# Performance work log

Measured on AMD Instinct MI355X. Metric: run time of the kernel, lower is better.

Reference implementation:

```python
import jax, jax.numpy as jnp
import numpy as np

EPS = 1e-12  # torch F.normalize eps


def setup_inputs() -> dict:
    key = jax.random.key(0)
    k1, k2, k3 = jax.random.split(key, 3)
    Bq, Lq, Bd, Ld, V, D = 32, 256, 32, 256, 768, 128
    qry_hidden = jax.random.normal(k1, (Bq, Lq, V), dtype=jnp.float32)
    doc_hidden = jax.random.normal(k2, (Bd, Ld, V), dtype=jnp.float32)
    W_tok = jax.random.normal(k3, (V, D), dtype=jnp.float32) * 0.02
    b_tok = jnp.zeros((D,), dtype=jnp.float32)
    qry_attention_mask = jnp.ones((Bq, Lq), dtype=jnp.int32)
    return {
        "qry_hidden": qry_hidden,
        "doc_hidden": doc_hidden,
        "W_tok": W_tok,
        "b_tok": b_tok,
        "qry_attention_mask": qry_attention_mask,
    }


def _tok_reps(hidden, W_tok, b_tok):
    # tok_proj + L2 normalize over feature dim (dim=2)
    r = hidden @ W_tok + b_tok
    norm = jnp.maximum(jnp.linalg.norm(r, axis=2, keepdims=True), EPS)
    return r / norm


def _mask_sep(mask):
    # zero out the [SEP] position (last 1 in each row)
    sep_pos = mask.sum(axis=1) - 1
    return mask.at[jnp.arange(mask.shape[0]), sep_pos].set(0)


def reference(qry_hidden, doc_hidden, W_tok, b_tok, qry_attention_mask):
    q = _tok_reps(qry_hidden, W_tok, b_tok)   # [Bq, Lq, D]
    d = _tok_reps(doc_hidden, W_tok, b_tok)   # [Bd, Ld, D]
    mask = _mask_sep(qry_attention_mask)      # [Bq, Lq]
    # cartesian token-level scores: [Bq, Lq, Bd, Ld], MaxSim over doc tokens
    scores = jnp.einsum("qld,bmd->qlbm", q, d).max(axis=3)  # [Bq, Lq, Bd]
    # masked sum over query tokens, skipping position 0 ([CLS])
    tok_scores = (scores * mask[:, :, None].astype(scores.dtype))[:, 1:].sum(axis=1)
    return tok_scores  # [Bq, Bd]
```

## Files before the change

### kernel.cpp

```cpp
#include <hip/hip_runtime.h>
#include <hip/hip_bf16.h>
#include <stdint.h>
#include <math.h>


#define BQ 32
#define LQ 256
#define V  768
#define DIM 128
#define NQ (BQ * LQ)
#define ND (BQ * LQ)

typedef short bf16x8 __attribute__((ext_vector_type(8)));
typedef float f32x4  __attribute__((ext_vector_type(4)));
typedef float f32x16 __attribute__((ext_vector_type(16)));
typedef float fvec4  __attribute__((ext_vector_type(4)));
typedef unsigned short us4 __attribute__((ext_vector_type(4)));

__device__ inline unsigned short f2bf(float f) {
  __hip_bfloat16 h = __float2bfloat16(f);
  unsigned short u;
  __builtin_memcpy(&u, &h, 2);
  return u;
}

__device__ inline void gload_lds16(const void* g, void* lds) {
  __builtin_amdgcn_global_load_lds(
      (const __attribute__((address_space(1))) void*)g,
      (__attribute__((address_space(3))) void*)lds, 16, 0, 0);
}

__global__ void prep_kernel(const float* __restrict__ W,
                            unsigned short* __restrict__ WT,
                            const int* __restrict__ mask,
                            float* __restrict__ wmask) {
  if (blockIdx.x < 384) {
    int idx = blockIdx.x * 256 + threadIdx.x;
    int n = idx & 127;
    int k = idx >> 7;
    float v = W[idx];
    int kg = k >> 6;
    int kc = k & 63;
    int wb = ((((kc >> 3) ^ (n & 7)) << 4) | ((kc & 7) << 1));
    *(unsigned short*)((char*)WT + (size_t)n * 1536 + kg * 128 + wb) = f2bf(v);
  } else {
    int b = blockIdx.x - 384, t = threadIdx.x;
    int m = mask[b * 256 + t];
    int s = m;
    #pragma unroll
    for (int off = 1; off < 64; off <<= 1) s += __shfl_xor(s, off, 64);
    __shared__ int ws[4];
    int w = t >> 6, l = t & 63;
    if (l == 0) ws[w] = s;
    __syncthreads();
    int total = ws[0] + ws[1] + ws[2] + ws[3];
    int sep = total - 1;
    float out = (t == 0 || t == sep) ? 0.0f : (float)m;
    wmask[b * 256 + t] = out;
  }
}

__launch_bounds__(256, 2)
__global__ void proj_kernel(const float* __restrict__ qh, const float* __restrict__ dh,
                            const unsigned short* __restrict__ WT,
                            const float* __restrict__ bias,
                            unsigned short* __restrict__ qrep,
                            unsigned short* __restrict__ drep) {
  __shared__ __align__(16) unsigned short At[2][32 * 64];
  __shared__ __align__(16) unsigned short Bt[2][128 * 64];
  __shared__ float sq[4][32];

  const int t = threadIdx.x;
  const int w = t >> 6;
  const int l = t & 63;
  const int lm = l & 15, lg = l >> 4;
  const int rowblk = blockIdx.x * 32;

  int arow[2], ac4[2];
  const float* asrc[2];
  #pragma unroll
  for (int p = 0; p < 2; p++) {
    int id = p * 256 + t;
    arow[p] = id >> 4;
    ac4[p] = id & 15;
    int row_g = rowblk + arow[p];
    asrc[p] = (row_g < NQ) ? (qh + (size_t)row_g * V)
                           : (dh + (size_t)(row_g - NQ) * V);
  }

  f32x4 acc[2][2];
  #pragma unroll
  for (int r = 0; r < 2; r++)
    #pragma unroll
    for (int c = 0; c < 2; c++)
      acc[r][c] = f32x4{0.f, 0.f, 0.f, 0.f};

  float bias_c[2];
  #pragma unroll
  for (int c = 0; c < 2; c++) bias_c[c] = bias[w * 32 + c * 16 + lm];

  fvec4 apref[2];
  #pragma unroll
  for (int p = 0; p < 2; p++) apref[p] = *(const fvec4*)(asrc[p] + ac4[p] * 4);
  #pragma unroll
  for (int i = 0; i < 4; i++) {
    int off = i * 4096 + t * 16;
    int n = off >> 7, inrow = off & 127;
    gload_lds16((const char*)WT + (size_t)n * 1536 + inrow,
                (char*)Bt[0] + i * 4096 + w * 1024);
  }
  #pragma unroll
  for (int p = 0; p < 2; p++) {
    us4 b4;
    #pragma unroll
    for (int j = 0; j < 4; j++) b4[j] = f2bf(apref[p][j]);
    int wb = ((((ac4[p] >> 1) ^ (arow[p] & 7)) << 4) | ((ac4[p] & 1) << 3));
    *(us4*)((char*)At[0] + arow[p] * 128 + wb) = b4;
  }
  __syncthreads();

  for (int kk = 0; kk < 12; kk++) {
    const int cur = kk & 1;
    if (kk < 11) {
      #pragma unroll
      for (int p = 0; p < 2; p++)
        apref[p] = *(const fvec4*)(asrc[p] + (kk + 1) * 64 + ac4[p] * 4);
      #pragma unroll
      for (int i = 0; i < 4; i++) {
        int off = i * 4096 + t * 16;
        int n = off >> 7, inrow = off & 127;
        gload_lds16((const char*)WT + (size_t)n * 1536 + (kk + 1) * 128 + inrow,
                    (char*)Bt[cur ^ 1] + i * 4096 + w * 1024);
      }
    }
    #pragma unroll
    for (int ks = 0; ks < 2; ks++) {
      bf16x8 af[2], bfr[2];
      #pragma unroll
      for (int r = 0; r < 2; r++) {
        int row = r * 16 + lm;
        int ch = (ks * 4 + lg) ^ (row & 7);
        af[r] = *(const bf16x8*)((char*)At[cur] + row * 128 + ch * 16);
      }
      #pragma unroll
      for (int c = 0; c < 2; c++) {
        int n = w * 32 + c * 16 + lm;
        int ch = (ks * 4 + lg) ^ (n & 7);
        bfr[c] = *(const bf16x8*)((char*)Bt[cur] + n * 128 + ch * 16);
      }
      #pragma unroll
      for (int r = 0; r < 2; r++)
        #pragma unroll
        for (int c = 0; c < 2; c++)
          acc[r][c] = __builtin_amdgcn_mfma_f32_16x16x32_bf16(af[r], bfr[c], acc[r][c], 0, 0, 0);
    }
    if (kk < 11) {
      #pragma unroll
      for (int p = 0; p < 2; p++) {
        us4 b4;
        #pragma unroll
        for (int j = 0; j < 4; j++) b4[j] = f2bf(apref[p][j]);
        int wb = ((((ac4[p] >> 1) ^ (arow[p] & 7)) << 4) | ((ac4[p] & 1) << 3));
        *(us4*)((char*)At[cur ^ 1] + arow[p] * 128 + wb) = b4;
      }
    }
    __syncthreads();
  }

  float vout[2][2][4];
  float ss[2][4];
  #pragma unroll
  for (int r = 0; r < 2; r++) {
    #pragma unroll
    for (int j = 0; j < 4; j++) {
      float s = 0.f;
      #pragma unroll
      for (int c = 0; c < 2; c++) {
        float v = acc[r][c][j] + bias_c[c];
        vout[r][c][j] = v;
        s += v * v;
      }
      #pragma unroll
      for (int m = 1; m < 16; m <<= 1) s += __shfl_xor(s, m, 64);
      ss[r][j] = s;
    }
  }
  if (lm == 0) {
    #pragma unroll
    for (int r = 0; r < 2; r++)
      #pragma unroll
      for (int j = 0; j < 4; j++)
        sq[w][r * 16 + lg * 4 + j] = ss[r][j];
  }
  __syncthreads();
  #pragma unroll
  for (int r = 0; r < 2; r++) {
    #pragma unroll
    for (int j = 0; j < 4; j++) {
      int rowl = r * 16 + lg * 4 + j;
      float tot = sq[0][rowl] + sq[1][rowl] + sq[2][rowl] + sq[3][rowl];
      float inv = 1.0f / fmaxf(sqrtf(tot), 1e-12f);
      int row_g = rowblk + rowl;
      unsigned short* rep = (row_g < NQ) ? qrep : drep;
      int rl = (row_g < NQ) ? row_g : row_g - NQ;
      #pragma unroll
      for (int c = 0; c < 2; c++) {
        int col = w * 32 + c * 16 + lm;
        int byteoff = rl * 256 + ((((col >> 3) ^ (rl & 15)) << 4) | ((col & 7) << 1));
        *(unsigned short*)((char*)rep + byteoff) = f2bf(vout[r][c][j] * inv);
      }
    }
  }
}

__launch_bounds__(512, 2)
__global__ void score_kernel(const unsigned short* __restrict__ qrep,
                             const unsigned short* __restrict__ drep,
                             const float* __restrict__ wmask,
                             float* __restrict__ out) {
  __shared__ __align__(16) char smem[131072];
  char* Qt  = smem;
  char* Dt0 = smem + 65536;
  char* Dt1 = smem + 98304;
  float* maxAll   = (float*)smem;
  float* partial2 = (float*)(smem + 8192);

  const int t = threadIdx.x;
  const int w = t >> 6, l = t & 63;
  const int col = l & 31, hi = l >> 5;
  const int wr = w >> 2, wc = w & 3;
  const int qb = blockIdx.x;
  const int dg = blockIdx.y;

  const char* qsrc = (const char*)qrep + (size_t)qb * 65536;
  const char* dsrc = (const char*)drep + (size_t)dg * 262144;

  #pragma unroll
  for (int i = 0; i < 8; i++)
    gload_lds16(qsrc + i * 8192 + t * 16, Qt + i * 8192 + w * 1024);
  #pragma unroll
  for (int i = 0; i < 4; i++)
    gload_lds16(dsrc + i * 8192 + t * 16, Dt0 + i * 8192 + w * 1024);
  __syncthreads();

  bf16x8 qf[2][8];
  #pragma unroll
  for (int c = 0; c < 2; c++) {
    int n = wc * 64 + c * 32 + col;
    const char* rowb = Qt + n * 256;
    #pragma unroll
    for (int ks = 0; ks < 8; ks++) {
      int ch = (ks * 2 + hi) ^ (n & 15);
      qf[c][ks] = *(const bf16x8*)(rowb + ch * 16);
    }
  }

  f32x16 acc[2][2];
  float vmax[2] = {-INFINITY, -INFINITY};

  for (int db = 0; db < 4; db++) {
    {
      const char* nsrc = dsrc + (size_t)(2 * db + 1) * 32768;
      #pragma unroll
      for (int i = 0; i < 4; i++)
        gload_lds16(nsrc + i * 8192 + t * 16, Dt1 + i * 8192 + w * 1024);
    }
    #pragma unroll
    for (int r = 0; r < 2; r++)
      #pragma unroll
      for (int c = 0; c < 2; c++)
        #pragma unroll
        for (int g = 0; g < 16; g++) acc[r][c][g] = 0.f;
    #pragma unroll
    for (int ks = 0; ks < 8; ks++) {
      bf16x8 df[2];
      #pragma unroll
      for (int r = 0; r < 2; r++) {
        int m = wr * 64 + r * 32 + col;
        int ch = (ks * 2 + hi) ^ (m & 15);
        df[r] = *(const bf16x8*)(Dt0 + m * 256 + ch * 16);
      }
      #pragma unroll
      for (int r = 0; r < 2; r++)
        #pragma unroll
        for (int c = 0; c < 2; c++)
          acc[r][c] = __builtin_amdgcn_mfma_f32_32x32x16_bf16(df[r], qf[c][ks], acc[r][c], 0, 0, 0);
    }
    #pragma unroll
    for (int c = 0; c < 2; c++)
      #pragma unroll
      for (int r = 0; r < 2; r++)
        #pragma unroll
        for (int g = 0; g < 16; g++) vmax[c] = fmaxf(vmax[c], acc[r][c][g]);
    __syncthreads();

    if (db < 3) {
      const char* nsrc = dsrc + (size_t)(2 * db + 2) * 32768;
      #pragma unroll
      for (int i = 0; i < 4; i++)
        gload_lds16(nsrc + i * 8192 + t * 16, Dt0 + i * 8192 + w * 1024);
    }
    #pragma unroll
    for (int r = 0; r < 2; r++)
      #pragma unroll
      for (int c = 0; c < 2; c++)
        #pragma unroll
        for (int g = 0; g < 16; g++) acc[r][c][g] = 0.f;
    #pragma unroll
    for (int ks = 0; ks < 8; ks++) {
      bf16x8 df[2];
      #pragma unroll
      for (int r = 0; r < 2; r++) {
        int m = wr * 64 + r * 32 + col;
        int ch = (ks * 2 + hi) ^ (m & 15);
        df[r] = *(const bf16x8*)(Dt1 + m * 256 + ch * 16);
      }
      #pragma unroll
      for (int r = 0; r < 2; r++)
        #pragma unroll
        for (int c = 0; c < 2; c++)
          acc[r][c] = __builtin_amdgcn_mfma_f32_32x32x16_bf16(df[r], qf[c][ks], acc[r][c], 0, 0, 0);
    }
    #pragma unroll
    for (int c = 0; c < 2; c++)
      #pragma unroll
      for (int r = 0; r < 2; r++)
        #pragma unroll
        for (int g = 0; g < 16; g++) vmax[c] = fmaxf(vmax[c], acc[r][c][g]);

    #pragma unroll
    for (int c = 0; c < 2; c++) {
      float m = vmax[c];
      m = fmaxf(m, __shfl_xor(m, 32, 64));
      if (hi == 0) maxAll[db * 512 + wr * 256 + wc * 64 + c * 32 + col] = m;
      vmax[c] = -INFINITY;
    }
    __syncthreads();
  }

  {
    int db = w >> 1, h = w & 1;
    int tok0 = h * 128 + l;
    int tok1 = tok0 + 64;
    float m0 = fmaxf(maxAll[db * 512 + tok0], maxAll[db * 512 + 256 + tok0]);
    float m1 = fmaxf(maxAll[db * 512 + tok1], maxAll[db * 512 + 256 + tok1]);
    float contrib = m0 * wmask[qb * 256 + tok0] + m1 * wmask[qb * 256 + tok1];
    #pragma unroll
    for (int off = 1; off < 64; off <<= 1) contrib += __shfl_xor(contrib, off, 64);
    if (l == 0) partial2[w] = contrib;
  }
  __syncthreads();
  if (t < 4)
    out[qb * 32 + dg * 4 + t] = partial2[2 * t] + partial2[2 * t + 1];
}

extern "C" void kernel_launch(void* const* d_in, const int* in_sizes, int n_in,
                              void* d_out, int out_size, void* d_ws, size_t ws_size,
                              hipStream_t stream) {
  const float* qh  = (const float*)d_in[0];
  const float* dh  = (const float*)d_in[1];
  const float* W   = (const float*)d_in[2];
  const float* b   = (const float*)d_in[3];
  const int* mask  = (const int*)d_in[4];
  float* out = (float*)d_out;

  char* ws = (char*)d_ws;
  unsigned short* qrep = (unsigned short*)(ws);
  unsigned short* drep = (unsigned short*)(ws + (1 << 21));
  unsigned short* WT   = (unsigned short*)(ws + (1 << 22));
  float* wmaskp        = (float*)(ws + (1 << 22) + (192 << 10));

  prep_kernel<<<416, 256, 0, stream>>>(W, WT, mask, wmaskp);
  proj_kernel<<<512, 256, 0, stream>>>(qh, dh, WT, b, qrep, drep);
  score_kernel<<<dim3(32, 8), 512, 0, stream>>>(qrep, drep, wmaskp, out);
}
```

Measured before the change: 118.5 us.

## Fuse prep, projection and scoring into one cooperative kernel with grid syncs

Merges the three kernels into a single cooperative launch of 256 blocks of 512 threads, separated by grid-wide barriers, to remove launch gaps between stages. The projection phase is retiled so each block handles 64 rows with a 128-wide K step instead of 32 rows with 64. The weighted mask is now computed inline in the scoring phase, and the separate mask buffer is dropped. In exchange, grid syncs add barrier cost, and the projection stage now runs on fewer, larger blocks, which lowers parallelism for the memory-bound read of the fp32 hidden states.

New measurement: 187.3 us. +58.0%, slower.

```diff
diff --git a/kernel.cpp b/kernel.cpp
--- a/kernel.cpp
+++ b/kernel.cpp
@@ -1,8 +1,11 @@
 #include <hip/hip_runtime.h>
+#include <hip/hip_cooperative_groups.h>
 #include <hip/hip_bf16.h>
 #include <stdint.h>
 #include <math.h>
 
+
+namespace cg = cooperative_groups;
 
 #define BQ 32
 #define LQ 256
@@ -30,328 +33,328 @@
       (__attribute__((address_space(3))) void*)lds, 16, 0, 0);
 }
 
-__global__ void prep_kernel(const float* __restrict__ W,
-                            unsigned short* __restrict__ WT,
-                            const int* __restrict__ mask,
-                            float* __restrict__ wmask) {
-  if (blockIdx.x < 384) {
-    int idx = blockIdx.x * 256 + threadIdx.x;
-    int n = idx & 127;
-    int k = idx >> 7;
-    float v = W[idx];
-    int kg = k >> 6;
-    int kc = k & 63;
-    int wb = ((((kc >> 3) ^ (n & 7)) << 4) | ((kc & 7) << 1));
-    *(unsigned short*)((char*)WT + (size_t)n * 1536 + kg * 128 + wb) = f2bf(v);
-  } else {
-    int b = blockIdx.x - 384, t = threadIdx.x;
-    int m = mask[b * 256 + t];
-    int s = m;
-    #pragma unroll
-    for (int off = 1; off < 64; off <<= 1) s += __shfl_xor(s, off, 64);
-    __shared__ int ws[4];
-    int w = t >> 6, l = t & 63;
-    if (l == 0) ws[w] = s;
+__launch_bounds__(512, 2)
+__global__ void colbert_fused(const float* __restrict__ qh,
+                              const float* __restrict__ dh,
+                              const float* __restrict__ W,
+                              const float* __restrict__ bias,
+                              const int* __restrict__ mask,
+                              unsigned short* __restrict__ WT,
+                              unsigned short* __restrict__ qrep,
+                              unsigned short* __restrict__ drep,
+                              float* __restrict__ out) {
+  __shared__ __align__(16) char smem[131072];
+  const int t = threadIdx.x;
+  const int blk = blockIdx.x;
+  const int w = t >> 6, l = t & 63;
+
+  {
+    int idx = blk * 512 + t;
+    if (idx < 98304) {
+      int n = idx & 127, k = idx >> 7;
+      float v = W[idx];
+      int kg = k >> 6, kc = k & 63;
+      int wb = ((((kc >> 3) ^ (n & 7)) << 4) | ((kc & 7) << 1));
+      *(unsigned short*)((char*)WT + (size_t)n * 1536 + kg * 128 + wb) = f2bf(v);
+    }
+  }
+  cg::this_grid().sync();
+
+  {
+    char* At = smem;
+    char* Bt = smem + 32768;
+    float* sq = (float*)(smem + 98304);
+    const int lm = l & 15, lg = l >> 4;
+    const int wr2 = w >> 2, wc = w & 3;
+    const int rowblk = blk * 64;
+
+    int arow[4], ac4[4];
+    const float* asrc[4];
+    #pragma unroll
+    for (int p = 0; p < 4; p++) {
+      int id = p * 512 + t;
+      arow[p] = id >> 5;
+      ac4[p]  = id & 31;
+      int row_g = rowblk + arow[p];
+      asrc[p] = (row_g < NQ) ? (qh + (size_t)row_g * V)
+                             : (dh + (size_t)(row_g - NQ) * V);
+    }
+
+    f32x4 acc[2][2];
+    #pragma unroll
+    for (int r = 0; r < 2; r++)
+      #pragma unroll
+      for (int c = 0; c < 2; c++)
+        acc[r][c] = f32x4{0.f, 0.f, 0.f, 0.f};
+
+    float bias_c[2];
+    #pragma unroll
+    for (int c = 0; c < 2; c++) bias_c[c] = bias[wc * 32 + c * 16 + lm];
+
+    fvec4 ap[4];
+    #pragma unroll
+    for (int p = 0; p < 4; p++) ap[p] = *(const fvec4*)(asrc[p] + ac4[p] * 4);
+    #pragma unroll
+    for (int i = 0; i < 4; i++) {
+      int off = i * 8192 + t * 16;
+      int h = off >> 14, offh = off & 16383;
+      int n = offh >> 7, inr = offh & 127;
+      gload_lds16((const char*)WT + (size_t)n * 1536 + h * 128 + inr, Bt + off);
+    }
+    #pragma unroll
+    for (int p = 0; p < 4; p++) {
+      us4 b4;
+      #pragma unroll
+      for (int j = 0; j < 4; j++) b4[j] = f2bf(ap[p][j]);
+      int h = ac4[p] >> 4, kc4 = ac4[p] & 15;
+      int wb = ((((kc4 >> 1) ^ (arow[p] & 7)) << 4) | ((kc4 & 1) << 3));
+      *(us4*)(At + h * 8192 + arow[p] * 128 + wb) = b4;
+    }
     __syncthreads();
-    int total = ws[0] + ws[1] + ws[2] + ws[3];
-    int sep = total - 1;
-    float out = (t == 0 || t == sep) ? 0.0f : (float)m;
-    wmask[b * 256 + t] = out;
+
+    for (int kk = 0; kk < 6; kk++) {
+      const int cur = kk & 1;
+      char* curA = At + cur * 16384;
+      char* curB = Bt + (cur << 15);
+      if (kk < 5) {
+        #pragma unroll
+        for (int p = 0; p < 4; p++)
+          ap[p] = *(const fvec4*)(asrc[p] + (kk + 1) * 128 + ac4[p] * 4);
+        char* nxtB = Bt + ((cur ^ 1) << 15);
+        #pragma unroll
+        for (int i = 0; i < 4; i++) {
+          int off = i * 8192 + t * 16;
+          int h = off >> 14, offh = off & 16383;
+          int n = offh >> 7, inr = offh & 127;
+          gload_lds16((const char*)WT + (size_t)n * 1536 + ((kk + 1) * 2 + h) * 128 + inr,
+                      nxtB + off);
+        }
+      }
+      #pragma unroll
+      for (int ks = 0; ks < 4; ks++) {
+        const int h = ks >> 1, ksl = ks & 1;
+        bf16x8 af[2], bfr[2];
+        #pragma unroll
+        for (int r = 0; r < 2; r++) {
+          int row = wr2 * 32 + r * 16 + lm;
+          int ch = (ksl * 4 + lg) ^ (row & 7);
+          af[r] = *(const bf16x8*)(curA + h * 8192 + row * 128 + ch * 16);
+        }
+        #pragma unroll
+        for (int c = 0; c < 2; c++) {
+          int n = wc * 32 + c * 16 + lm;
+          int ch = (ksl * 4 + lg) ^ (n & 7);
+          bfr[c] = *(const bf16x8*)(curB + h * 16384 + n * 128 + ch * 16);
+        }
+        #pragma unroll
+        for (int r = 0; r < 2; r++)
+          #pragma unroll
+          for (int c = 0; c < 2; c++)
+            acc[r][c] = __builtin_amdgcn_mfma_f32_16x16x32_bf16(af[r], bfr[c], acc[r][c], 0, 0, 0);
+      }
+      if (kk < 5) {
+        char* nxtA = At + (cur ^ 1) * 16384;
+        #pragma unroll
+        for (int p = 0; p < 4; p++) {
+          us4 b4;
+          #pragma unroll
+          for (int j = 0; j < 4; j++) b4[j] = f2bf(ap[p][j]);
+          int h = ac4[p] >> 4, kc4 = ac4[p] & 15;
+          int wb = ((((kc4 >> 1) ^ (arow[p] & 7)) << 4) | ((kc4 & 1) << 3));
+          *(us4*)(nxtA + h * 8192 + arow[p] * 128 + wb) = b4;
+        }
+      }
+      __syncthreads();
+    }
+
+    float vout[2][2][4];
+    float ss[2][4];
+    #pragma unroll
+    for (int r = 0; r < 2; r++) {
+      #pragma unroll
+      for (int j = 0; j < 4; j++) {
+        float s = 0.f;
+        #pragma unroll
+        for (int c = 0; c < 2; c++) {
+          float v = acc[r][c][j] + bias_c[c];
+          vout[r][c][j] = v;
+          s += v * v;
+        }
+        #pragma unroll
+        for (int m = 1; m < 16; m <<= 1) s += __shfl_xor(s, m, 64);
+        ss[r][j] = s;
+      }
+    }
+    if (lm == 0) {
+      #pragma unroll
+      for (int r = 0; r < 2; r++)
+        #pragma unroll
+        for (int j = 0; j < 4; j++)
+          sq[wc * 64 + wr2 * 32 + r * 16 + lg * 4 + j] = ss[r][j];
+    }
+    __syncthreads();
+    #pragma unroll
+    for (int r = 0; r < 2; r++) {
+      #pragma unroll
+      for (int j = 0; j < 4; j++) {
+        int brow = wr2 * 32 + r * 16 + lg * 4 + j;
+        float tot = sq[brow] + sq[64 + brow] + sq[128 + brow] + sq[192 + brow];
+        float inv = 1.0f / fmaxf(sqrtf(tot), 1e-12f);
+        int row_g = rowblk + brow;
+        unsigned short* rep = (row_g < NQ) ? qrep : drep;
+        int rl = (row_g < NQ) ? row_g : row_g - NQ;
+        #pragma unroll
+        for (int c = 0; c < 2; c++) {
+          int col = wc * 32 + c * 16 + lm;
+          int byteoff = rl * 256 + ((((col >> 3) ^ (rl & 15)) << 4) | ((col & 7) << 1));
+          *(unsigned short*)((char*)rep + byteoff) = f2bf(vout[r][c][j] * inv);
+        }
+      }
+    }
   }
-}
-
-__launch_bounds__(256, 2)
-__global__ void proj_kernel(const float* __restrict__ qh, const float* __restrict__ dh,
-                            const unsigned short* __restrict__ WT,
-                            const float* __restrict__ bias,
-                            unsigned short* __restrict__ qrep,
-                            unsigned short* __restrict__ drep) {
-  __shared__ __align__(16) unsigned short At[2][32 * 64];
-  __shared__ __align__(16) unsigned short Bt[2][128 * 64];
-  __shared__ float sq[4][32];
-
-  const int t = threadIdx.x;
-  const int w = t >> 6;
-  const int l = t & 63;
-  const int lm = l & 15, lg = l >> 4;
-  const int rowblk = blockIdx.x * 32;
-
-  int arow[2], ac4[2];
-  const float* asrc[2];
-  #pragma unroll
-  for (int p = 0; p < 2; p++) {
-    int id = p * 256 + t;
-    arow[p] = id >> 4;
-    ac4[p] = id & 15;
-    int row_g = rowblk + arow[p];
-    asrc[p] = (row_g < NQ) ? (qh + (size_t)row_g * V)
-                           : (dh + (size_t)(row_g - NQ) * V);
+  cg::this_grid().sync();
+
+  {
+    char* Qt  = smem;
+    char* Dt0 = smem + 65536;
+    char* Dt1 = smem + 98304;
+    float* maxAll   = (float*)smem;
+    float* partial2 = (float*)(smem + 8192);
+
+    const int col = l & 31, hi = l >> 5;
+    const int wr = w >> 2, wc = w & 3;
+    const int qb = blk >> 3;
+    const int dg = blk & 7;
+
+    const char* qsrc = (const char*)qrep + (size_t)qb * 65536;
+    const char* dsrc = (const char*)drep + (size_t)dg * 262144;
+
+    #pragma unroll
+    for (int i = 0; i < 8; i++)
+      gload_lds16(qsrc + i * 8192 + t * 16, Qt + i * 8192 + w * 1024);
+    #pragma unroll
+    for (int i = 0; i < 4; i++)
+      gload_lds16(dsrc + i * 8192 + t * 16, Dt0 + i * 8192 + w * 1024);
+    __syncthreads();
+
+    bf16x8 qf[2][8];
+    #pragma unroll
+    for (int c = 0; c < 2; c++) {
+      int n = wc * 64 + c * 32 + col;
+      const char* rowb = Qt + n * 256;
+      #pragma unroll
+      for (int ks = 0; ks < 8; ks++) {
+        int ch = (ks * 2 + hi) ^ (n & 15);
+        qf[c][ks] = *(const bf16x8*)(rowb + ch * 16);
+      }
+    }
+
+    f32x16 acc[2][2];
+    float vmax[2] = {-INFINITY, -INFINITY};
+
+    for (int db = 0; db < 4; db++) {
+      {
+        const char* nsrc = dsrc + (size_t)(2 * db + 1) * 32768;
+        #pragma unroll
+        for (int i = 0; i < 4; i++)
+          gload_lds16(nsrc + i * 8192 + t * 16, Dt1 + i * 8192 + w * 1024);
+      }
+      #pragma unroll
+      for (int r = 0; r < 2; r++)
+        #pragma unroll
+        for (int c = 0; c < 2; c++)
+          #pragma unroll
+          for (int g = 0; g < 16; g++) acc[r][c][g] = 0.f;
+      #pragma unroll
+      for (int ks = 0; ks < 8; ks++) {
+        bf16x8 df[2];
+        #pragma unroll
+        for (int r = 0; r < 2; r++) {
+          int m = wr * 64 + r * 32 + col;
+          int ch = (ks * 2 + hi) ^ (m & 15);
+          df[r] = *(const bf16x8*)(Dt0 + m * 256 + ch * 16);
+        }
+        #pragma unroll
+        for (int r = 0; r < 2; r++)
+          #pragma unroll
+          for (int c = 0; c < 2; c++)
+            acc[r][c] = __builtin_amdgcn_mfma_f32_32x32x16_bf16(df[r], qf[c][ks], acc[r][c], 0, 0, 0);
+      }
+      #pragma unroll
+      for (int c = 0; c < 2; c++)
+        #pragma unroll
+        for (int r = 0; r < 2; r++)
+          #pragma unroll
+          for (int g = 0; g < 16; g++) vmax[c] = fmaxf(vmax[c], acc[r][c][g]);
+      __syncthreads();
+
+      if (db < 3) {
+        const char* nsrc = dsrc + (size_t)(2 * db + 2) * 32768;
+        #pragma unroll
+        for (int i = 0; i < 4; i++)
+          gload_lds16(nsrc + i * 8192 + t * 16, Dt0 + i * 8192 + w * 1024);
+      }
+      #pragma unroll
+      for (int r = 0; r < 2; r++)
+        #pragma unroll
+        for (int c = 0; c < 2; c++)
+          #pragma unroll
+          for (int g = 0; g < 16; g++) acc[r][c][g] = 0.f;
+      #pragma unroll
+      for (int ks = 0; ks < 8; ks++) {
+        bf16x8 df[2];
+        #pragma unroll
+        for (int r = 0; r < 2; r++) {
+          int m = wr * 64 + r * 32 + col;
+          int ch = (ks * 2 + hi) ^ (m & 15);
+          df[r] = *(const bf16x8*)(Dt1 + m * 256 + ch * 16);
+        }
+        #pragma unroll
+        for (int r = 0; r < 2; r++)
+          #pragma unroll
+          for (int c = 0; c < 2; c++)
+            acc[r][c] = __builtin_amdgcn_mfma_f32_32x32x16_bf16(df[r], qf[c][ks], acc[r][c], 0, 0, 0);
+      }
+      #pragma unroll
+      for (int c = 0; c < 2; c++)
+        #pragma unroll
+        for (int r = 0; r < 2; r++)
+          #pragma unroll
+          for (int g = 0; g < 16; g++) vmax[c] = fmaxf(vmax[c], acc[r][c][g]);
+
+      #pragma unroll
+      for (int c = 0; c < 2; c++) {
+        float m = vmax[c];
+        m = fmaxf(m, __shfl_xor(m, 32, 64));
+        if (hi == 0) maxAll[db * 512 + wr * 256 + wc * 64 + c * 32 + col] = m;
+        vmax[c] = -INFINITY;
+      }
+      __syncthreads();
+    }
+
+    {
+      int s = 0;
+      #pragma unroll
+      for (int p = 0; p < 4; p++) s += mask[qb * 256 + p * 64 + l];
+      #pragma unroll
+      for (int off = 1; off < 64; off <<= 1) s += __shfl_xor(s, off, 64);
+      int sep = s - 1;
+      int db = w >> 1, h = w & 1;
+      int tok0 = h * 128 + l;
+      int tok1 = tok0 + 64;
+      float m0 = fmaxf(maxAll[db * 512 + tok0], maxAll[db * 512 + 256 + tok0]);
+      float m1 = fmaxf(maxAll[db * 512 + tok1], maxAll[db * 512 + 256 + tok1]);
+      float wm0 = (tok0 != 0 && tok0 != sep) ? (float)mask[qb * 256 + tok0] : 0.f;
+      float wm1 = (tok1 != 0 && tok1 != sep) ? (float)mask[qb * 256 + tok1] : 0.f;
+      float contrib = m0 * wm0 + m1 * wm1;
+      #pragma unroll
+      for (int off = 1; off < 64; off <<= 1) contrib += __shfl_xor(contrib, off, 64);
+      if (l == 0) partial2[w] = contrib;
+    }
+    __syncthreads();
+    if (t < 4)
+      out[qb * 32 + dg * 4 + t] = partial2[2 * t] + partial2[2 * t + 1];
   }
-
-  f32x4 acc[2][2];
-  #pragma unroll
-  for (int r = 0; r < 2; r++)
-    #pragma unroll
-    for (int c = 0; c < 2; c++)
-      acc[r][c] = f32x4{0.f, 0.f, 0.f, 0.f};
-
-  float bias_c[2];
-  #pragma unroll
-  for (int c = 0; c < 2; c++) bias_c[c] = bias[w * 32 + c * 16 + lm];
-
-  fvec4 apref[2];
-  #pragma unroll
-  for (int p = 0; p < 2; p++) apref[p] = *(const fvec4*)(asrc[p] + ac4[p] * 4);
-  #pragma unroll
-  for (int i = 0; i < 4; i++) {
-    int off = i * 4096 + t * 16;
-    int n = off >> 7, inrow = off & 127;
-    gload_lds16((const char*)WT + (size_t)n * 1536 + inrow,
-                (char*)Bt[0] + i * 4096 + w * 1024);
-  }
-  #pragma unroll
-  for (int p = 0; p < 2; p++) {
-    us4 b4;
-    #pragma unroll
-    for (int j = 0; j < 4; j++) b4[j] = f2bf(apref[p][j]);
-    int wb = ((((ac4[p] >> 1) ^ (arow[p] & 7)) << 4) | ((ac4[p] & 1) << 3));
-    *(us4*)((char*)At[0] + arow[p] * 128 + wb) = b4;
-  }
-  __syncthreads();
-
-  for (int kk = 0; kk < 12; kk++) {
-    const int cur = kk & 1;
-    if (kk < 11) {
-      #pragma unroll
-      for (int p = 0; p < 2; p++)
-        apref[p] = *(const fvec4*)(asrc[p] + (kk + 1) * 64 + ac4[p] * 4);
-      #pragma unroll
-      for (int i = 0; i < 4; i++) {
-        int off = i * 4096 + t * 16;
-        int n = off >> 7, inrow = off & 127;
-        gload_lds16((const char*)WT + (size_t)n * 1536 + (kk + 1) * 128 + inrow,
-                    (char*)Bt[cur ^ 1] + i * 4096 + w * 1024);
-      }
-    }
-    #pragma unroll
-    for (int ks = 0; ks < 2; ks++) {
-      bf16x8 af[2], bfr[2];
-      #pragma unroll
-      for (int r = 0; r < 2; r++) {
-        int row = r * 16 + lm;
-        int ch = (ks * 4 + lg) ^ (row & 7);
-        af[r] = *(const bf16x8*)((char*)At[cur] + row * 128 + ch * 16);
-      }
-      #pragma unroll
-      for (int c = 0; c < 2; c++) {
-        int n = w * 32 + c * 16 + lm;
-        int ch = (ks * 4 + lg) ^ (n & 7);
-        bfr[c] = *(const bf16x8*)((char*)Bt[cur] + n * 128 + ch * 16);
-      }
-      #pragma unroll
-      for (int r = 0; r < 2; r++)
-        #pragma unroll
-        for (int c = 0; c < 2; c++)
-          acc[r][c] = __builtin_amdgcn_mfma_f32_16x16x32_bf16(af[r], bfr[c], acc[r][c], 0, 0, 0);
-    }
-    if (kk < 11) {
-      #pragma unroll
-      for (int p = 0; p < 2; p++) {
-        us4 b4;
-        #pragma unroll
-        for (int j = 0; j < 4; j++) b4[j] = f2bf(apref[p][j]);
-        int wb = ((((ac4[p] >> 1) ^ (arow[p] & 7)) << 4) | ((ac4[p] & 1) << 3));
-        *(us4*)((char*)At[cur ^ 1] + arow[p] * 128 + wb) = b4;
-      }
-    }
-    __syncthreads();
-  }
-
-  float vout[2][2][4];
-  float ss[2][4];
-  #pragma unroll
-  for (int r = 0; r < 2; r++) {
-    #pragma unroll
-    for (int j = 0; j < 4; j++) {
-      float s = 0.f;
-      #pragma unroll
-      for (int c = 0; c < 2; c++) {
-        float v = acc[r][c][j] + bias_c[c];
-        vout[r][c][j] = v;
-        s += v * v;
-      }
-      #pragma unroll
-      for (int m = 1; m < 16; m <<= 1) s += __shfl_xor(s, m, 64);
-      ss[r][j] = s;
-    }
-  }
-  if (lm == 0) {
-    #pragma unroll
-    for (int r = 0; r < 2; r++)
-      #pragma unroll
-      for (int j = 0; j < 4; j++)
-        sq[w][r * 16 + lg * 4 + j] = ss[r][j];
-  }
-  __syncthreads();
-  #pragma unroll
-  for (int r = 0; r < 2; r++) {
-    #pragma unroll
-    for (int j = 0; j < 4; j++) {
-      int rowl = r * 16 + lg * 4 + j;
-      float tot = sq[0][rowl] + sq[1][rowl] + sq[2][rowl] + sq[3][rowl];
-      float inv = 1.0f / fmaxf(sqrtf(tot), 1e-12f);
-      int row_g = rowblk + rowl;
-      unsigned short* rep = (row_g < NQ) ? qrep : drep;
-      int rl = (row_g < NQ) ? row_g : row_g - NQ;
-      #pragma unroll
-      for (int c = 0; c < 2; c++) {
-        int col = w * 32 + c * 16 + lm;
-        int byteoff = rl * 256 + ((((col >> 3) ^ (rl & 15)) << 4) | ((col & 7) << 1));
-        *(unsigned short*)((char*)rep + byteoff) = f2bf(vout[r][c][j] * inv);
-      }
-    }
-  }
-}
-
-__launch_bounds__(512, 2)
-__global__ void score_kernel(const unsigned short* __restrict__ qrep,
-                             const unsigned short* __restrict__ drep,
-                             const float* __restrict__ wmask,
-                             float* __restrict__ out) {
-  __shared__ __align__(16) char smem[131072];
-  char* Qt  = smem;
-  char* Dt0 = smem + 65536;
-  char* Dt1 = smem + 98304;
-  float* maxAll   = (float*)smem;
-  float* partial2 = (float*)(smem + 8192);
-
-  const int t = threadIdx.x;
-  const int w = t >> 6, l = t & 63;
-  const int col = l & 31, hi = l >> 5;
-  const int wr = w >> 2, wc = w & 3;
-  const int qb = blockIdx.x;
-  const int dg = blockIdx.y;
-
-  const char* qsrc = (const char*)qrep + (size_t)qb * 65536;
-  const char* dsrc = (const char*)drep + (size_t)dg * 262144;
-
-  #pragma unroll
-  for (int i = 0; i < 8; i++)
-    gload_lds16(qsrc + i * 8192 + t * 16, Qt + i * 8192 + w * 1024);
-  #pragma unroll
-  for (int i = 0; i < 4; i++)
-    gload_lds16(dsrc + i * 8192 + t * 16, Dt0 + i * 8192 + w * 1024);
-  __syncthreads();
-
-  bf16x8 qf[2][8];
-  #pragma unroll
-  for (int c = 0; c < 2; c++) {
-    int n = wc * 64 + c * 32 + col;
-    const char* rowb = Qt + n * 256;
-    #pragma unroll
-    for (int ks = 0; ks < 8; ks++) {
-      int ch = (ks * 2 + hi) ^ (n & 15);
-      qf[c][ks] = *(const bf16x8*)(rowb + ch * 16);
-    }
-  }
-
-  f32x16 acc[2][2];
-  float vmax[2] = {-INFINITY, -INFINITY};
-
-  for (int db = 0; db < 4; db++) {
-    {
-      const char* nsrc = dsrc + (size_t)(2 * db + 1) * 32768;
-      #pragma unroll
-      for (int i = 0; i < 4; i++)
-        gload_lds16(nsrc + i * 8192 + t * 16, Dt1 + i * 8192 + w * 1024);
-    }
-    #pragma unroll
-    for (int r = 0; r < 2; r++)
-      #pragma unroll
-      for (int c = 0; c < 2; c++)
-        #pragma unroll
-        for (int g = 0; g < 16; g++) acc[r][c][g] = 0.f;
-    #pragma unroll
-    for (int ks = 0; ks < 8; ks++) {
-      bf16x8 df[2];
-      #pragma unroll
-      for (int r = 0; r < 2; r++) {
-        int m = wr * 64 + r * 32 + col;
-        int ch = (ks * 2 + hi) ^ (m & 15);
-        df[r] = *(const bf16x8*)(Dt0 + m * 256 + ch * 16);
-      }
-      #pragma unroll
-      for (int r = 0; r < 2; r++)
-        #pragma unroll
-        for (int c = 0; c < 2; c++)
-          acc[r][c] = __builtin_amdgcn_mfma_f32_32x32x16_bf16(df[r], qf[c][ks], acc[r][c], 0, 0, 0);
-    }
-    #pragma unroll
-    for (int c = 0; c < 2; c++)
-      #pragma unroll
-      for (int r = 0; r < 2; r++)
-        #pragma unroll
-        for (int g = 0; g < 16; g++) vmax[c] = fmaxf(vmax[c], acc[r][c][g]);
-    __syncthreads();
-
-    if (db < 3) {
-      const char* nsrc = dsrc + (size_t)(2 * db + 2) * 32768;
-      #pragma unroll
-      for (int i = 0; i < 4; i++)
-        gload_lds16(nsrc + i * 8192 + t * 16, Dt0 + i * 8192 + w * 1024);
-    }
-    #pragma unroll
-    for (int r = 0; r < 2; r++)
-      #pragma unroll
-      for (int c = 0; c < 2; c++)
-        #pragma unroll
-        for (int g = 0; g < 16; g++) acc[r][c][g] = 0.f;
-    #pragma unroll
-    for (int ks = 0; ks < 8; ks++) {
-      bf16x8 df[2];
-      #pragma unroll
-      for (int r = 0; r < 2; r++) {
-        int m = wr * 64 + r * 32 + col;
-        int ch = (ks * 2 + hi) ^ (m & 15);
-        df[r] = *(const bf16x8*)(Dt1 + m * 256 + ch * 16);
-      }
-      #pragma unroll
-      for (int r = 0; r < 2; r++)
-        #pragma unroll
-        for (int c = 0; c < 2; c++)
-          acc[r][c] = __builtin_amdgcn_mfma_f32_32x32x16_bf16(df[r], qf[c][ks], acc[r][c], 0, 0, 0);
-    }
-    #pragma unroll
-    for (int c = 0; c < 2; c++)
-      #pragma unroll
-      for (int r = 0; r < 2; r++)
-        #pragma unroll
-        for (int g = 0; g < 16; g++) vmax[c] = fmaxf(vmax[c], acc[r][c][g]);
-
-    #pragma unroll
-    for (int c = 0; c < 2; c++) {
-      float m = vmax[c];
-      m = fmaxf(m, __shfl_xor(m, 32, 64));
-      if (hi == 0) maxAll[db * 512 + wr * 256 + wc * 64 + c * 32 + col] = m;
-      vmax[c] = -INFINITY;
-    }
-    __syncthreads();
-  }
-
-  {
-    int db = w >> 1, h = w & 1;
-    int tok0 = h * 128 + l;
-    int tok1 = tok0 + 64;
-    float m0 = fmaxf(maxAll[db * 512 + tok0], maxAll[db * 512 + 256 + tok0]);
-    float m1 = fmaxf(maxAll[db * 512 + tok1], maxAll[db * 512 + 256 + tok1]);
-    float contrib = m0 * wmask[qb * 256 + tok0] + m1 * wmask[qb * 256 + tok1];
-    #pragma unroll
-    for (int off = 1; off < 64; off <<= 1) contrib += __shfl_xor(contrib, off, 64);
-    if (l == 0) partial2[w] = contrib;
-  }
-  __syncthreads();
-  if (t < 4)
-    out[qb * 32 + dg * 4 + t] = partial2[2 * t] + partial2[2 * t + 1];
 }
 
 extern "C" void kernel_launch(void* const* d_in, const int* in_sizes, int n_in,
@@ -368,9 +371,9 @@
   unsigned short* qrep = (unsigned short*)(ws);
   unsigned short* drep = (unsigned short*)(ws + (1 << 21));
   unsigned short* WT   = (unsigned short*)(ws + (1 << 22));
-  float* wmaskp        = (float*)(ws + (1 << 22) + (192 << 10));
-
-  prep_kernel<<<416, 256, 0, stream>>>(W, WT, mask, wmaskp);
-  proj_kernel<<<512, 256, 0, stream>>>(qh, dh, WT, b, qrep, drep);
-  score_kernel<<<dim3(32, 8), 512, 0, stream>>>(qrep, drep, wmaskp, out);
+
+  void* args[] = {(void*)&qh, (void*)&dh, (void*)&W, (void*)&b, (void*)&mask,
+                  (void*)&WT, (void*)&qrep, (void*)&drep, (void*)&out};
+  hipLaunchCooperativeKernel((const void*)colbert_fused, dim3(256), dim3(512),
+                             args, 0, stream);
 }
```
